# Kernel optimization log

Hardware: AMD Instinct MI355X
Metric: run time of the kernel (lower is better)

The kernel has to match this reference:

```python
import jax, jax.numpy as jnp
import numpy as np

B, W, N, F_IN = 2, 8, 10000, 5
E = 80000
H = 128


def setup_inputs() -> dict:
    key = jax.random.key(0)
    ks = jax.random.split(key, 16)
    s = 0.05
    inp = {
        "x": jax.random.normal(ks[0], (B, W, N, F_IN), dtype=jnp.float32),
        "edge_index": jax.random.randint(ks[1], (2, E), 0, N, dtype=jnp.int64),
        # GCN layer 1 (in_features -> hidden) and layer 2 (hidden -> hidden)
        "gcn1_w": jax.random.normal(ks[2], (F_IN, H), dtype=jnp.float32) * s,
        "gcn1_b": jnp.zeros((H,), dtype=jnp.float32),
        "gcn2_w": jax.random.normal(ks[3], (H, H), dtype=jnp.float32) * s,
        "gcn2_b": jnp.zeros((H,), dtype=jnp.float32),
        # LSTM (torch gate order: i, f, g, o)
        "lstm_w_ih": jax.random.normal(ks[4], (4 * H, H), dtype=jnp.float32) * s,
        "lstm_w_hh": jax.random.normal(ks[5], (4 * H, H), dtype=jnp.float32) * s,
        "lstm_b_ih": jnp.zeros((4 * H,), dtype=jnp.float32),
        "lstm_b_hh": jnp.zeros((4 * H,), dtype=jnp.float32),
        # Decoder MLP: H -> H//2 -> 1
        "dec_w1": jax.random.normal(ks[6], (H, H // 2), dtype=jnp.float32) * s,
        "dec_b1": jnp.zeros((H // 2,), dtype=jnp.float32),
        "dec_w2": jax.random.normal(ks[7], (H // 2, 1), dtype=jnp.float32) * s,
        "dec_b2": jnp.zeros((1,), dtype=jnp.float32),
    }
    return inp


def _forward(x, edge_index, gcn1_w, gcn1_b, gcn2_w, gcn2_b,
             lstm_w_ih, lstm_w_hh, lstm_b_ih, lstm_b_hh,
             dec_w1, dec_b1, dec_w2, dec_b2):
    b, w, n, f_in = x.shape
    h_dim = gcn1_w.shape[1]
    # --- GCN normalization (PyG GCNConv default: add self-loops, sym-norm) ---
    loop = jnp.arange(n, dtype=edge_index.dtype)
    src = jnp.concatenate([edge_index[0], loop])
    dst = jnp.concatenate([edge_index[1], loop])
    deg = jnp.zeros((n,), x.dtype).at[dst].add(jnp.float32(1.0))
    dinv = jax.lax.rsqrt(deg)
    norm = dinv[src] * dinv[dst]  # (E+N,)

    def gcn(h, wm, bias):
        # h: (BW, N, Fin) -> (BW, N, H). Transform-then-aggregate (linear op).
        ht = h @ wm                                   # (BW, N, H)
        msg = ht[:, src, :] * norm[None, :, None]      # (BW, E+N, H)
        agg = jnp.zeros_like(ht).at[:, dst, :].add(msg)
        return agg + bias

    xf = x.reshape(b * w, n, f_in)
    h = jax.nn.relu(gcn(xf, gcn1_w, gcn1_b))   # dropout is identity at eval
    h = jax.nn.relu(gcn(h, gcn2_w, gcn2_b))

    # (BW, N, H) -> (B, N, W, H) -> (B*N, W, H): per-node temporal sequences
    h = h.reshape(b, w, n, h_dim).transpose(0, 2, 1, 3).reshape(b * n, w, h_dim)

    # --- single-layer LSTM, keep only last hidden state ---
    def step(carry, xt):
        hp, cp = carry
        gates = xt @ lstm_w_ih.T + hp @ lstm_w_hh.T + lstm_b_ih + lstm_b_hh
        i, f, g, o = jnp.split(gates, 4, axis=-1)
        c = jax.nn.sigmoid(f) * cp + jax.nn.sigmoid(i) * jnp.tanh(g)
        hn = jax.nn.sigmoid(o) * jnp.tanh(c)
        return (hn, c), None

    init = (jnp.zeros((b * n, h_dim), x.dtype), jnp.zeros((b * n, h_dim), x.dtype))
    (h_last, _), _ = jax.lax.scan(step, init, h.transpose(1, 0, 2))  # scan over W

    # --- MLP decoder ---
    d = jax.nn.relu(h_last @ dec_w1 + dec_b1)
    pred = (d @ dec_w2 + dec_b2)[..., 0]
    return pred.reshape(b, n)


def reference(x, edge_index, gcn1_w, gcn1_b, gcn2_w, gcn2_b,
              lstm_w_ih, lstm_w_hh, lstm_b_ih, lstm_b_hh,
              dec_w1, dec_b1, dec_w2, dec_b2):
    return _forward(x, edge_index, gcn1_w, gcn1_b, gcn2_w, gcn2_b,
                    lstm_w_ih, lstm_w_hh, lstm_b_ih, lstm_b_hh,
                    dec_w1, dec_b1, dec_w2, dec_b2)
```

## Files before the change

kernel.cpp:

```cpp
#include <hip/hip_runtime.h>
#include <hip/hip_fp16.h>
#include <cstdint>
#include <cstddef>

#define Bn   2
#define Wn   8
#define Nn   10000
#define Fin  5
#define En   80000
#define Hn   128
#define BWn  (Bn*Wn)
#define ROWS (BWn*Nn)
#define MR   (Bn*Nn)
#define LROWS 32

typedef _Float16 half8 __attribute__((ext_vector_type(8)));
typedef float f32x4 __attribute__((ext_vector_type(4)));

#define LOG2E 1.44269504088896f

__device__ __forceinline__ float fast_sigmoid(float x) {
    return __builtin_amdgcn_rcpf(1.f + __builtin_amdgcn_exp2f(-LOG2E * x));
}
__device__ __forceinline__ float fast_tanh(float x) {
    return fmaf(-2.f, __builtin_amdgcn_rcpf(1.f + __builtin_amdgcn_exp2f(2.f * LOG2E * x)), 1.f);
}

__global__ __launch_bounds__(256) void setup_kernel(
    const int* __restrict__ ei, const float* __restrict__ bih, const float* __restrict__ bhh,
    const float* __restrict__ wih, const float* __restrict__ whh,
    const float* __restrict__ g2w, const float* __restrict__ x,
    const float* __restrict__ dw1,
    int* __restrict__ counts, float* __restrict__ bsum,
    _Float16* __restrict__ wif, _Float16* __restrict__ whf,
    _Float16* __restrict__ g2wt, float* __restrict__ xt,
    _Float16* __restrict__ d1f) {
    __shared__ float buf[6400];
    const int b = blockIdx.x;
    const int tid = threadIdx.x;
    if (b < 313) {
        int e = b * 256 + tid;
        if (e < En) atomicAdd(&counts[ei[En + e]], 1);
    } else if (b < 315) {
        int i = (b - 313) * 256 + tid;
        if (i < 4 * Hn) bsum[i] = bih[i] + bhh[i];
    } else if (b < 891) {
        int i = (b - 315) * 256 + tid;
        if (i < 131072) {
            int idx = i & 65535;
            int j = idx & 7, lane = (idx >> 3) & 63, kt = (idx >> 9) & 3, ct = idx >> 11;
            int n = ct * 16 + (lane & 15);
            int k = kt * 32 + (lane >> 4) * 8 + j;
            if (i < 65536) wif[idx] = (_Float16)wih[n * 128 + k];
            else           whf[idx] = (_Float16)whh[n * 128 + k];
        } else {
            int j = i - 131072;
            int n = j >> 7, k = j & 127;
            g2wt[j] = (_Float16)g2w[k * Hn + n];
        }
    } else if (b < 1016) {
        const int n0 = (b - 891) * 80;
        for (int i = tid; i < 6400; i += 256) {
            int s = i / 400, r = i - s * 400;
            int node = r / 5, f = r - node * 5;
            buf[(node * 16 + s) * 5 + f] = x[((size_t)s * Nn + n0) * 5 + r];
        }
        __syncthreads();
        float* dst = xt + (size_t)n0 * 80;
        for (int i = tid; i < 6400; i += 256) dst[i] = buf[i];
    } else {
        int i = (b - 1016) * 256 + tid;
        int j = i & 7, lane = (i >> 3) & 63, kt = (i >> 9) & 3, ct = i >> 11;
        int n = ct * 16 + (lane & 15);
        int k = kt * 32 + (lane >> 4) * 8 + j;
        d1f[i] = (_Float16)dw1[k * 64 + n];
    }
}

enum { CHUNK = 10 };
static_assert(CHUNK * 1024 >= Nn, "scan chunk");

__global__ __launch_bounds__(1024) void scan_kernel(
    const int* __restrict__ counts, int* __restrict__ row_ptr,
    int* __restrict__ fill_ptr, float* __restrict__ dinv) {
    __shared__ int sums[1024];
    const int t = threadIdx.x;
    const int base = t * CHUNK;
    int cnt[CHUNK];
    int s = 0;
    #pragma unroll
    for (int i = 0; i < CHUNK; ++i) {
        int idx = base + i;
        int v = (idx < Nn) ? counts[idx] + 1 : 0;
        cnt[i] = v; s += v;
    }
    sums[t] = s;
    __syncthreads();
    for (int off = 1; off < 1024; off <<= 1) {
        int v = (t >= off) ? sums[t - off] : 0;
        __syncthreads();
        sums[t] += v;
        __syncthreads();
    }
    int excl = (t == 0) ? 0 : sums[t - 1];
    #pragma unroll
    for (int i = 0; i < CHUNK; ++i) {
        int idx = base + i;
        if (idx < Nn) {
            row_ptr[idx] = excl;
            fill_ptr[idx] = excl;
            dinv[idx] = rsqrtf((float)cnt[i]);
            excl += cnt[i];
        }
    }
    if (t == 1023) row_ptr[Nn] = excl;
}

__global__ void fill_kernel(const int* __restrict__ ei,
                            const float* __restrict__ dinv,
                            int* fill_ptr, int* __restrict__ col,
                            float* __restrict__ wgt) {
    int i = blockIdx.x * blockDim.x + threadIdx.x;
    if (i < Nn) {
        int p = atomicAdd(&fill_ptr[i], 1);
        col[p] = i;
        wgt[p] = dinv[i] * dinv[i];
    } else if (i < Nn + En) {
        int e = i - Nn;
        int s = ei[e];
        int d = ei[En + e];
        int p = atomicAdd(&fill_ptr[d], 1);
        col[p] = s;
        wgt[p] = dinv[s] * dinv[d];
    }
}

__global__ __launch_bounds__(128) void agg_x_kernel(
    const float* __restrict__ xt, const int* __restrict__ row_ptr,
    const int* __restrict__ col, const float* __restrict__ wgt,
    float* __restrict__ aggx) {
    const int n = blockIdx.x;
    const int t = threadIdx.x;
    const int s = t >> 3, f = t & 7;
    if (f >= Fin) return;
    const int start = row_ptr[n], end = row_ptr[n + 1];
    const int off = s * 5 + f;
    float acc0 = 0.f, acc1 = 0.f;
    int e = start;
    for (; e + 1 < end; e += 2) {
        int c0 = col[e], c1 = col[e + 1];
        float w0 = wgt[e], w1 = wgt[e + 1];
        float v0 = xt[(size_t)c0 * 80 + off];
        float v1 = xt[(size_t)c1 * 80 + off];
        acc0 = fmaf(w0, v0, acc0);
        acc1 = fmaf(w1, v1, acc1);
    }
    if (e < end) acc0 = fmaf(wgt[e], xt[(size_t)col[e] * 80 + off], acc0);
    aggx[(size_t)n * 80 + off] = acc0 + acc1;
}

__global__ __launch_bounds__(256) void gcn2_fused_kernel(
    const float* __restrict__ aggx, const float* __restrict__ w1,
    const float* __restrict__ b1, const _Float16* __restrict__ g2wt,
    _Float16* __restrict__ C) {
    __shared__ __align__(16) _Float16 s_buf[128][136];
    __shared__ _Float16 Bs[128][40];
    const int tid = threadIdx.x;
    const int m0 = blockIdx.x * 128;
    {
        const int rg = tid >> 4;
        const int cg = tid & 15;
        float wreg[Fin][8], breg[8];
        #pragma unroll
        for (int k = 0; k < 8; ++k) breg[k] = b1[cg * 8 + k];
        #pragma unroll
        for (int f = 0; f < Fin; ++f)
            #pragma unroll
            for (int k = 0; k < 8; ++k) wreg[f][k] = w1[f * Hn + cg * 8 + k];
        #pragma unroll
        for (int rr = 0; rr < 8; ++rr) {
            const float* ar = aggx + (size_t)(m0 + rg * 8 + rr) * Fin;
            float a[Fin];
            #pragma unroll
            for (int f = 0; f < Fin; ++f) a[f] = ar[f];
            half8 v;
            #pragma unroll
            for (int k = 0; k < 8; ++k) {
                float s = breg[k];
                #pragma unroll
                for (int f = 0; f < Fin; ++f) s = fmaf(a[f], wreg[f][k], s);
                v[k] = (_Float16)fmaxf(s, 0.f);
            }
            *(half8*)&s_buf[rg * 8 + rr][cg * 8] = v;
        }
    }
    __syncthreads();
    const int wave = tid >> 6, lane = tid & 63;
    const int l = lane & 15, q = lane >> 4;
    const int wm = (wave & 1) * 64, wn = (wave >> 1) * 64;
    f32x4 acc[4][4];
    #pragma unroll
    for (int i = 0; i < 4; ++i)
        #pragma unroll
        for (int j = 0; j < 4; ++j) acc[i][j] = (f32x4){0.f, 0.f, 0.f, 0.f};
    for (int kt = 0; kt < 128; kt += 32) {
        #pragma unroll
        for (int j = 0; j < 2; ++j) {
            int idx = tid + j * 256;
            int r = idx >> 2, c = (idx & 3) * 8;
            *(half8*)&Bs[r][c] = *(const half8*)(g2wt + (size_t)r * 128 + kt + c);
        }
        __syncthreads();
        half8 af[4], bf[4];
        #pragma unroll
        for (int i = 0; i < 4; ++i) af[i] = *(const half8*)&s_buf[wm + i * 16 + l][kt + q * 8];
        #pragma unroll
        for (int j = 0; j < 4; ++j) bf[j] = *(const half8*)&Bs[wn + j * 16 + l][q * 8];
        #pragma unroll
        for (int i = 0; i < 4; ++i)
            #pragma unroll
            for (int j = 0; j < 4; ++j)
                acc[i][j] = __builtin_amdgcn_mfma_f32_16x16x32_f16(
                    af[i], bf[j], acc[i][j], 0, 0, 0);
        __syncthreads();
    }
    #pragma unroll
    for (int j = 0; j < 4; ++j) {
        int ccol = wn + j * 16 + l;
        #pragma unroll
        for (int i = 0; i < 4; ++i)
            #pragma unroll
            for (int r = 0; r < 4; ++r)
                s_buf[wm + i * 16 + q * 4 + r][ccol] = (_Float16)acc[i][j][r];
    }
    __syncthreads();
    const size_t base = (size_t)m0 * 128;
    #pragma unroll
    for (int it = 0; it < 8; ++it) {
        int idx = it * 256 + tid;
        int row = idx >> 4, ch = (idx & 15) * 8;
        *(half8*)(C + base + (size_t)row * 128 + ch) = *(const half8*)&s_buf[row][ch];
    }
}

__global__ __launch_bounds__(128) void gcn_agg2_kernel(
    const _Float16* __restrict__ ht, const int* __restrict__ row_ptr,
    const int* __restrict__ col, const float* __restrict__ wgt,
    const float* __restrict__ bias, _Float16* __restrict__ out) {
    const int n = blockIdx.x;
    const int t = threadIdx.x;
    const int s = blockIdx.y * 8 + (t >> 4);
    const int g = (t & 15) * 8;
    const int start = row_ptr[n], end = row_ptr[n + 1];
    const size_t lofs = (size_t)s * Hn + g;
    float acc[8];
    #pragma unroll
    for (int j = 0; j < 8; ++j) acc[j] = 0.f;
    int e = start;
    for (; e + 3 < end; e += 4) {
        const int c0 = col[e], c1 = col[e + 1], c2 = col[e + 2], c3 = col[e + 3];
        const float w0 = wgt[e], w1 = wgt[e + 1], w2 = wgt[e + 2], w3 = wgt[e + 3];
        half8 v0 = *(const half8*)(ht + (size_t)c0 * (BWn * Hn) + lofs);
        half8 v1 = *(const half8*)(ht + (size_t)c1 * (BWn * Hn) + lofs);
        half8 v2 = *(const half8*)(ht + (size_t)c2 * (BWn * Hn) + lofs);
        half8 v3 = *(const half8*)(ht + (size_t)c3 * (BWn * Hn) + lofs);
        #pragma unroll
        for (int j = 0; j < 8; ++j) {
            acc[j] = fmaf(w0, (float)v0[j], acc[j]);
            acc[j] = fmaf(w1, (float)v1[j], acc[j]);
            acc[j] = fmaf(w2, (float)v2[j], acc[j]);
            acc[j] = fmaf(w3, (float)v3[j], acc[j]);
        }
    }
    for (; e < end; ++e) {
        const float w = wgt[e];
        half8 v = *(const half8*)(ht + (size_t)col[e] * (BWn * Hn) + lofs);
        #pragma unroll
        for (int j = 0; j < 8; ++j) acc[j] = fmaf(w, (float)v[j], acc[j]);
    }
    half8 o;
    #pragma unroll
    for (int j = 0; j < 8; ++j) o[j] = (_Float16)fmaxf(acc[j] + bias[g + j], 0.f);
    *(half8*)(out + (size_t)n * (BWn * Hn) + lofs) = o;
}

__global__ __launch_bounds__(512, 1) void lstm_fused6_kernel(
    const _Float16* __restrict__ h2, const _Float16* __restrict__ wif,
    const _Float16* __restrict__ whf, const float* __restrict__ bsum,
    const _Float16* __restrict__ d1f, const float* __restrict__ db1,
    const float* __restrict__ dw2, const float* __restrict__ db2,
    float* __restrict__ out) {
    __shared__ __align__(16) _Float16 x_lds[2][LROWS][144];
    __shared__ __align__(16) _Float16 h_lds[2][LROWS][144];
    const int tid = threadIdx.x;
    const int nw = tid >> 6, lane = tid & 63;
    const int l = lane & 15, q = lane >> 4;
    const int r0 = blockIdx.x * LROWS;
    const int srow = tid >> 4, sch = (tid & 15) * 8;
    const int sgrow = r0 + srow;
    const int sb = (sgrow >= Nn) ? 1 : 0;
    const int sn = sgrow - sb * Nn;
    const _Float16* xbase = h2 + ((size_t)sn * BWn + sb * Wn) * 128 + sch;

    half8 wic[4][4], whc[4][4];
    #pragma unroll
    for (int g = 0; g < 4; ++g) {
        int ct = g * 8 + nw;
        #pragma unroll
        for (int kt = 0; kt < 4; ++kt) {
            wic[g][kt] = *(const half8*)(wif + (((size_t)ct * 4 + kt) * 64 + lane) * 8);
            whc[g][kt] = *(const half8*)(whf + (((size_t)ct * 4 + kt) * 64 + lane) * 8);
        }
    }
    float bias[4];
    #pragma unroll
    for (int g = 0; g < 4; ++g) bias[g] = bsum[g * 128 + nw * 16 + l];
    float c_reg[2][4];
    #pragma unroll
    for (int i = 0; i < 2; ++i)
        #pragma unroll
        for (int r = 0; r < 4; ++r) c_reg[i][r] = 0.f;

    *(half8*)&x_lds[0][srow][sch] = *(const half8*)(xbase);
    __syncthreads();

    for (int t = 0; t < Wn; ++t) {
        half8 xv = {0, 0, 0, 0, 0, 0, 0, 0};
        if (t + 1 < Wn) xv = *(const half8*)(xbase + (size_t)(t + 1) * 128);

        f32x4 acc[2][4];
        #pragma unroll
        for (int i = 0; i < 2; ++i)
            #pragma unroll
            for (int g = 0; g < 4; ++g)
                acc[i][g] = (f32x4){bias[g], bias[g], bias[g], bias[g]};

        #pragma unroll
        for (int kt = 0; kt < 4; ++kt) {
            half8 af[2];
            #pragma unroll
            for (int i = 0; i < 2; ++i)
                af[i] = *(const half8*)&x_lds[t & 1][i * 16 + l][kt * 32 + q * 8];
            #pragma unroll
            for (int i = 0; i < 2; ++i)
                #pragma unroll
                for (int g = 0; g < 4; ++g)
                    acc[i][g] = __builtin_amdgcn_mfma_f32_16x16x32_f16(
                        af[i], wic[g][kt], acc[i][g], 0, 0, 0);
        }
        if (t > 0) {
            #pragma unroll
            for (int kt = 0; kt < 4; ++kt) {
                half8 af[2];
                #pragma unroll
                for (int i = 0; i < 2; ++i)
                    af[i] = *(const half8*)&h_lds[t & 1][i * 16 + l][kt * 32 + q * 8];
                #pragma unroll
                for (int i = 0; i < 2; ++i)
                    #pragma unroll
                    for (int g = 0; g < 4; ++g)
                        acc[i][g] = __builtin_amdgcn_mfma_f32_16x16x32_f16(
                            af[i], whc[g][kt], acc[i][g], 0, 0, 0);
            }
        }

        #pragma unroll
        for (int i = 0; i < 2; ++i) {
            #pragma unroll
            for (int r = 0; r < 4; ++r) {
                float si = fast_sigmoid(acc[i][0][r]);
                float sf = fast_sigmoid(acc[i][1][r]);
                float tg = fast_tanh(acc[i][2][r]);
                float so = fast_sigmoid(acc[i][3][r]);
                float cn = sf * c_reg[i][r] + si * tg;
                c_reg[i][r] = cn;
                h_lds[(t + 1) & 1][i * 16 + q * 4 + r][nw * 16 + l] =
                    (_Float16)(so * fast_tanh(cn));
            }
        }
        if (t + 1 < Wn) *(half8*)&x_lds[(t + 1) & 1][srow][sch] = xv;
        __syncthreads();
    }

    const int mi = nw >> 2;
    const int ni = nw & 3;
    f32x4 dacc = (f32x4){0.f, 0.f, 0.f, 0.f};
    #pragma unroll
    for (int kt = 0; kt < 4; ++kt) {
        half8 af = *(const half8*)&h_lds[0][mi * 16 + l][kt * 32 + q * 8];
        half8 bf = *(const half8*)(d1f + (((size_t)ni * 4 + kt) * 64 + lane) * 8);
        dacc = __builtin_amdgcn_mfma_f32_16x16x32_f16(af, bf, dacc, 0, 0, 0);
    }
    const int unit = ni * 16 + l;
    const float bd1 = db1[unit];
    const float wd2 = dw2[unit];
    float pr[4];
    #pragma unroll
    for (int r = 0; r < 4; ++r)
        pr[r] = fmaxf(dacc[r] + bd1, 0.f) * wd2;
    #pragma unroll
    for (int m = 1; m < 16; m <<= 1)
        #pragma unroll
        for (int r = 0; r < 4; ++r)
            pr[r] += __shfl_xor(pr[r], m);
    float* part = (float*)&x_lds[0][0][0];
    if (l == 0) {
        #pragma unroll
        for (int r = 0; r < 4; ++r)
            part[(mi * 16 + q * 4 + r) * 4 + ni] = pr[r];
    }
    __syncthreads();
    if (tid < LROWS) {
        float s = part[tid * 4] + part[tid * 4 + 1] + part[tid * 4 + 2] + part[tid * 4 + 3];
        out[r0 + tid] = s + db2[0];
    }
}


extern "C" void kernel_launch(void* const* d_in, const int* in_sizes, int n_in,
                              void* d_out, int out_size, void* d_ws, size_t ws_size,
                              hipStream_t stream) {
    const float* x   = (const float*)d_in[0];
    const int*   ei  = (const int*)d_in[1];
    const float* g1w = (const float*)d_in[2];
    const float* g1b = (const float*)d_in[3];
    const float* g2w = (const float*)d_in[4];
    const float* g2b = (const float*)d_in[5];
    const float* wih = (const float*)d_in[6];
    const float* whh = (const float*)d_in[7];
    const float* bih = (const float*)d_in[8];
    const float* bhh = (const float*)d_in[9];
    const float* dw1 = (const float*)d_in[10];
    const float* db1 = (const float*)d_in[11];
    const float* dw2 = (const float*)d_in[12];
    const float* db2 = (const float*)d_in[13];
    float* out = (float*)d_out;

    char* p = (char*)d_ws;
    auto alloc = [&](size_t bytes) {
        char* r = p;
        p += (bytes + 255) & ~(size_t)255;
        return r;
    };
    int*      counts   = (int*)     alloc(Nn * 4);
    int*      row_ptr  = (int*)     alloc((Nn + 1) * 4);
    int*      fill_ptr = (int*)     alloc((Nn + 1) * 4);
    float*    dinv     = (float*)   alloc(Nn * 4);
    float*    bsum     = (float*)   alloc(4 * Hn * 4);
    int*      col      = (int*)     alloc((En + Nn) * 4);
    float*    wgt      = (float*)   alloc((En + Nn) * 4);
    _Float16* wif      = (_Float16*)alloc(512 * 128 * 2);
    _Float16* whf      = (_Float16*)alloc(512 * 128 * 2);
    _Float16* g2wt     = (_Float16*)alloc(128 * 128 * 2);
    _Float16* d1f      = (_Float16*)alloc(64 * 128 * 2);
    float*    xt       = (float*)   alloc((size_t)Nn * 80 * 4);
    float*    aggx     = (float*)   alloc((size_t)ROWS * Fin * 4);
    _Float16* htf      = (_Float16*)alloc((size_t)ROWS * Hn * 2);
    _Float16* h2f      = (_Float16*)alloc((size_t)ROWS * Hn * 2);

    hipMemsetAsync(counts, 0, Nn * 4, stream);

    setup_kernel<<<1048, 256, 0, stream>>>(ei, bih, bhh, wih, whh, g2w, x, dw1,
                                           counts, bsum, wif, whf, g2wt, xt, d1f);
    scan_kernel<<<1, 1024, 0, stream>>>(counts, row_ptr, fill_ptr, dinv);
    fill_kernel<<<(Nn + En + 255) / 256, 256, 0, stream>>>(ei, dinv, fill_ptr, col, wgt);

    agg_x_kernel<<<Nn, 128, 0, stream>>>(xt, row_ptr, col, wgt, aggx);

    gcn2_fused_kernel<<<ROWS / 128, 256, 0, stream>>>(aggx, g1w, g1b, g2wt, htf);

    gcn_agg2_kernel<<<dim3(Nn, 2), 128, 0, stream>>>(htf, row_ptr, col, wgt, g2b, h2f);

    lstm_fused6_kernel<<<MR / LROWS, 512, 0, stream>>>(
        h2f, wif, whf, bsum, d1f, db1, dw2, db2, out);
}
```

Measured before the change: 245.6 us.

## Fuse layer-1 feature aggregation into GCN2 GEMM kernel and shrink agg2 blocks

Removes the separate agg_x kernel and performs the 5-feature neighbor aggregation for a block's 8 nodes directly inside gcn2_fused_kernel, staging the result in LDS. This drops one launch and the aggx global round trip. It also halves the gcn_agg2 block size to 64 threads with a 4-way grid split to raise block count. The fused aggregation uses one 32-thread group per node, so load imbalance on high-degree nodes can now stall the GEMM block.

```diff
diff --git a/kernel.cpp b/kernel.cpp
--- a/kernel.cpp
+++ b/kernel.cpp
@@ -135,38 +135,35 @@
     }
 }
 
-__global__ __launch_bounds__(128) void agg_x_kernel(
+__global__ __launch_bounds__(256) void gcn2_fused_kernel(
     const float* __restrict__ xt, const int* __restrict__ row_ptr,
     const int* __restrict__ col, const float* __restrict__ wgt,
-    float* __restrict__ aggx) {
-    const int n = blockIdx.x;
-    const int t = threadIdx.x;
-    const int s = t >> 3, f = t & 7;
-    if (f >= Fin) return;
-    const int start = row_ptr[n], end = row_ptr[n + 1];
-    const int off = s * 5 + f;
-    float acc0 = 0.f, acc1 = 0.f;
-    int e = start;
-    for (; e + 1 < end; e += 2) {
-        int c0 = col[e], c1 = col[e + 1];
-        float w0 = wgt[e], w1 = wgt[e + 1];
-        float v0 = xt[(size_t)c0 * 80 + off];
-        float v1 = xt[(size_t)c1 * 80 + off];
-        acc0 = fmaf(w0, v0, acc0);
-        acc1 = fmaf(w1, v1, acc1);
-    }
-    if (e < end) acc0 = fmaf(wgt[e], xt[(size_t)col[e] * 80 + off], acc0);
-    aggx[(size_t)n * 80 + off] = acc0 + acc1;
-}
-
-__global__ __launch_bounds__(256) void gcn2_fused_kernel(
-    const float* __restrict__ aggx, const float* __restrict__ w1,
-    const float* __restrict__ b1, const _Float16* __restrict__ g2wt,
-    _Float16* __restrict__ C) {
+    const float* __restrict__ w1, const float* __restrict__ b1,
+    const _Float16* __restrict__ g2wt, _Float16* __restrict__ C) {
+    __shared__ float agg_lds[128 * 5];
     __shared__ __align__(16) _Float16 s_buf[128][136];
     __shared__ _Float16 Bs[128][40];
     const int tid = threadIdx.x;
     const int m0 = blockIdx.x * 128;
+    const int n0 = m0 >> 4;
+    {
+        const int nl = tid >> 5;
+        const int it = tid & 31;
+        const int n = n0 + nl;
+        const int start = row_ptr[n], end = row_ptr[n + 1];
+        float a0 = 0.f, a1 = 0.f, a2 = 0.f;
+        for (int e = start; e < end; ++e) {
+            const float w = wgt[e];
+            const float* src = xt + (size_t)col[e] * 80;
+            a0 = fmaf(w, src[it], a0);
+            a1 = fmaf(w, src[it + 32], a1);
+            if (it < 16) a2 = fmaf(w, src[it + 64], a2);
+        }
+        agg_lds[nl * 80 + it] = a0;
+        agg_lds[nl * 80 + it + 32] = a1;
+        if (it < 16) agg_lds[nl * 80 + it + 64] = a2;
+    }
+    __syncthreads();
     {
         const int rg = tid >> 4;
         const int cg = tid & 15;
@@ -179,7 +176,7 @@
             for (int k = 0; k < 8; ++k) wreg[f][k] = w1[f * Hn + cg * 8 + k];
         #pragma unroll
         for (int rr = 0; rr < 8; ++rr) {
-            const float* ar = aggx + (size_t)(m0 + rg * 8 + rr) * Fin;
+            const float* ar = &agg_lds[(rg * 8 + rr) * Fin];
             float a[Fin];
             #pragma unroll
             for (int f = 0; f < Fin; ++f) a[f] = ar[f];
@@ -243,13 +240,13 @@
     }
 }
 
-__global__ __launch_bounds__(128) void gcn_agg2_kernel(
+__global__ __launch_bounds__(64) void gcn_agg2_kernel(
     const _Float16* __restrict__ ht, const int* __restrict__ row_ptr,
     const int* __restrict__ col, const float* __restrict__ wgt,
     const float* __restrict__ bias, _Float16* __restrict__ out) {
     const int n = blockIdx.x;
     const int t = threadIdx.x;
-    const int s = blockIdx.y * 8 + (t >> 4);
+    const int s = blockIdx.y * 4 + (t >> 4);
     const int g = (t & 15) * 8;
     const int start = row_ptr[n], end = row_ptr[n + 1];
     const size_t lofs = (size_t)s * Hn + g;
@@ -454,7 +451,6 @@
     _Float16* g2wt     = (_Float16*)alloc(128 * 128 * 2);
     _Float16* d1f      = (_Float16*)alloc(64 * 128 * 2);
     float*    xt       = (float*)   alloc((size_t)Nn * 80 * 4);
-    float*    aggx     = (float*)   alloc((size_t)ROWS * Fin * 4);
     _Float16* htf      = (_Float16*)alloc((size_t)ROWS * Hn * 2);
     _Float16* h2f      = (_Float16*)alloc((size_t)ROWS * Hn * 2);
 
@@ -465,11 +461,10 @@
     scan_kernel<<<1, 1024, 0, stream>>>(counts, row_ptr, fill_ptr, dinv);
     fill_kernel<<<(Nn + En + 255) / 256, 256, 0, stream>>>(ei, dinv, fill_ptr, col, wgt);
 
-    agg_x_kernel<<<Nn, 128, 0, stream>>>(xt, row_ptr, col, wgt, aggx);
-
-    gcn2_fused_kernel<<<ROWS / 128, 256, 0, stream>>>(aggx, g1w, g1b, g2wt, htf);
-
-    gcn_agg2_kernel<<<dim3(Nn, 2), 128, 0, stream>>>(htf, row_ptr, col, wgt, g2b, h2f);
+    gcn2_fused_kernel<<<ROWS / 128, 256, 0, stream>>>(
+        xt, row_ptr, col, wgt, g1w, g1b, g2wt, htf);
+
+    gcn_agg2_kernel<<<dim3(Nn, 4), 64, 0, stream>>>(htf, row_ptr, col, wgt, g2b, h2f);
 
     lstm_fused6_kernel<<<MR / LROWS, 512, 0, stream>>>(
         h2f, wif, whf, bsum, d1f, db1, dw2, db2, out);
```

Result: no change. 245.3 us, median of 3 (-0.2%).
